# Kernel optimization log

Measured on AMD Instinct MI355X. Metric: run time of the kernel, lower is better.

The kernel has to match this reference:

```python
import jax, jax.numpy as jnp
import numpy as np

DIM = 1024
MLP_RATIO = 4
EPS = 1e-6


def rmsnorm(x, w):
    return x * jax.lax.rsqrt(jnp.mean(x * x, axis=-1, keepdims=True) + EPS) * w


def film(x, cond, w, b):
    # cond: [B, D] -> scale/shift: [B, D] each, broadcast over tokens
    ss = cond @ w + b  # [B, 2D]
    scale, shift = jnp.split(ss, 2, axis=-1)
    return x * (1.0 + scale[:, None, :]) + shift[:, None, :]


def setup_inputs() -> dict:
    key = jax.random.key(0)
    ks = jax.random.split(key, 16)
    B, N, D = 4, 2048, DIM
    H = D * MLP_RATIO
    s = lambda fan_in: 1.0 / np.sqrt(fan_in)
    return {
        "x": jax.random.normal(ks[0], (B, N, D), jnp.float32),
        "cond": jax.random.normal(ks[1], (B, D), jnp.float32),
        "norm1_w": jnp.ones((D,), jnp.float32),
        "film1_w": jax.random.normal(ks[2], (D, 2 * D), jnp.float32) * s(D),
        "film1_b": jnp.zeros((2 * D,), jnp.float32),
        "q_w": jax.random.normal(ks[3], (D, D), jnp.float32) * s(D),
        "q_b": jnp.zeros((D,), jnp.float32),
        "k_w": jax.random.normal(ks[4], (D, D), jnp.float32) * s(D),
        "k_b": jnp.zeros((D,), jnp.float32),
        "v_w": jax.random.normal(ks[5], (D, D), jnp.float32) * s(D),
        "v_b": jnp.zeros((D,), jnp.float32),
        "proj_w": jax.random.normal(ks[6], (D, D), jnp.float32) * s(D),
        "proj_b": jnp.zeros((D,), jnp.float32),
        "norm2_w": jnp.ones((D,), jnp.float32),
        "film2_w": jax.random.normal(ks[7], (D, 2 * D), jnp.float32) * s(D),
        "film2_b": jnp.zeros((2 * D,), jnp.float32),
        "mlp_w1": jax.random.normal(ks[8], (D, H), jnp.float32) * s(D),
        "mlp_b1": jnp.zeros((H,), jnp.float32),
        "mlp_w2": jax.random.normal(ks[9], (H, D), jnp.float32) * s(H),
        "mlp_b2": jnp.zeros((D,), jnp.float32),
    }


def reference(x, cond, norm1_w, film1_w, film1_b, q_w, q_b, k_w, k_b, v_w, v_b,
              proj_w, proj_b, norm2_w, film2_w, film2_b, mlp_w1, mlp_b1,
              mlp_w2, mlp_b2):
    B, N, D = x.shape
    x_in = x
    h = film(rmsnorm(x, norm1_w), cond, film1_w, film1_b)
    Q = h @ q_w + q_b
    K = h @ k_w + k_b
    V = h @ v_w + v_b
    scores = jnp.einsum('bnd,bmd->bnm', Q, K) * (D ** -0.5)  # [B,N,N]
    attn = jax.nn.softmax(scores, axis=-1)
    out = jnp.einsum('bnm,bmd->bnd', attn, V)
    x = x_in + (out @ proj_w + proj_b)
    x_in = x
    h = film(rmsnorm(x, norm2_w), cond, film2_w, film2_b)
    h = jax.nn.gelu(h @ mlp_w1 + mlp_b1, approximate=False) @ mlp_w2 + mlp_b2
    return x_in + h
```

## Files before the change

### kernel.cpp

```cpp
#include <hip/hip_runtime.h>
#include <math.h>

typedef unsigned short u16;
typedef unsigned int u32;
typedef __bf16 bf16;
typedef bf16 bf16x8 __attribute__((ext_vector_type(8)));
typedef float f32x4 __attribute__((ext_vector_type(4)));

#define DEV __device__ __forceinline__
#define MFMA(a, b, c) __builtin_amdgcn_mfma_f32_16x16x32_bf16(a, b, c, 0, 0, 0)

DEV u16 f2b(float f) {
  unsigned u = __builtin_bit_cast(unsigned, f);
  u += 0x7fffu + ((u >> 16) & 1u);
  return (u16)(u >> 16);
}
DEV float b2f(u16 h) {
  unsigned u = ((unsigned)h) << 16;
  return __builtin_bit_cast(float, u);
}
DEV float gelu_f(float x) {
  float e = __expf(x * (-1.5957691216f - 0.07135481283f * x * x));
  return x / (1.0f + e);
}

DEV void gl2lds16(const void* g, void* l) {
  __builtin_amdgcn_global_load_lds(
      (const __attribute__((address_space(1))) unsigned int*)g,
      (__attribute__((address_space(3))) unsigned int*)l, 16, 0, 0);
}

struct TDesc { const float* src; u16* dst; int R, C, t0, tx; };
struct T6 { TDesc d[6]; };

__global__ void k_transpose6(T6 td) {
  __shared__ float tile[32][33];
  const int id = blockIdx.x;
  TDesc d = td.d[0];
#pragma unroll
  for (int k = 1; k < 6; ++k)
    if (id >= td.d[k].t0) d = td.d[k];
  const int local = id - d.t0;
  const int c0 = (local % d.tx) * 32, r0 = (local / d.tx) * 32;
  const int tx = threadIdx.x, ty = threadIdx.y;
#pragma unroll
  for (int i = 0; i < 32; i += 8)
    tile[ty + i][tx] = d.src[(long)(r0 + ty + i) * d.C + c0 + tx];
  __syncthreads();
#pragma unroll
  for (int i = 0; i < 32; i += 8)
    d.dst[(long)(c0 + ty + i) * d.R + r0 + tx] = f2b(tile[tx][ty + i]);
}

__global__ __launch_bounds__(256) void k_film_part(const float* __restrict__ cond,
                                                   const float* __restrict__ f1w,
                                                   const float* __restrict__ f2w,
                                                   float* __restrict__ part) {
  const int j = blockIdx.x * 256 + threadIdx.x;
  const int b = blockIdx.y;
  const int z = blockIdx.z;
  const int kz = z & 7;
  const float* fw = (z < 8) ? f1w : f2w;
  const float* cp = cond + b * 1024 + kz * 128;
  const float* wp = fw + (long)kz * 128 * 2048 + j;
  float acc = 0.0f;
#pragma unroll 4
  for (int d = 0; d < 128; ++d) acc = fmaf(cp[d], wp[(long)d * 2048], acc);
  part[((z * 4 + b) << 11) + j] = acc;
}
__global__ __launch_bounds__(256) void k_film_comb(const float* __restrict__ part,
                                                   const float* __restrict__ f1b,
                                                   const float* __restrict__ f2b_,
                                                   float* __restrict__ ss) {
  const int j = blockIdx.x * 256 + threadIdx.x;
  const int b = blockIdx.y & 3, f = blockIdx.y >> 2;
  float a = (f ? f2b_ : f1b)[j];
#pragma unroll
  for (int kz = 0; kz < 8; ++kz) a += part[(((f * 8 + kz) * 4 + b) << 11) + j];
  ss[((f * 4 + b) << 11) + j] = a;
}

template <typename InT>
__global__ __launch_bounds__(256) void k_rmsfilm(const InT* __restrict__ x,
                                                 const float* __restrict__ nw,
                                                 const float* __restrict__ ss,
                                                 u16* __restrict__ h) {
  const int row = blockIdx.x;
  const int b = row >> 11;
  const int t = threadIdx.x;
  float4 v;
  if constexpr (sizeof(InT) == 4) {
    v = ((const float4*)(x + (long)row * 1024))[t];
  } else {
    ushort4 u = ((const ushort4*)(x + (long)row * 1024))[t];
    v = make_float4(b2f(u.x), b2f(u.y), b2f(u.z), b2f(u.w));
  }
  float s = v.x * v.x + v.y * v.y + v.z * v.z + v.w * v.w;
#pragma unroll
  for (int off = 32; off; off >>= 1) s += __shfl_xor(s, off);
  __shared__ float red[4];
  const int wv = t >> 6, lane = t & 63;
  if (lane == 0) red[wv] = s;
  __syncthreads();
  const float tot = red[0] + red[1] + red[2] + red[3];
  const float rn = rsqrtf(tot * (1.0f / 1024.0f) + 1e-6f);
  const float4 w4 = ((const float4*)nw)[t];
  const float4 sc = ((const float4*)(ss + b * 2048))[t];
  const float4 sh = ((const float4*)(ss + b * 2048 + 1024))[t];
  ushort4 o;
  o.x = f2b(v.x * rn * w4.x * (1.0f + sc.x) + sh.x);
  o.y = f2b(v.y * rn * w4.y * (1.0f + sc.y) + sh.y);
  o.z = f2b(v.z * rn * w4.z * (1.0f + sc.z) + sh.z);
  o.w = f2b(v.w * rn * w4.w * (1.0f + sc.w) + sh.w);
  ((ushort4*)(h + (long)row * 1024))[t] = o;
}

__global__ __launch_bounds__(256) void k_rowsuminv(const float* __restrict__ part,
                                                   float* __restrict__ inv) {
  const int id = blockIdx.x * 256 + threadIdx.x;
  float s = 0.0f;
#pragma unroll
  for (int b = 0; b < 16; ++b) s += part[b * 8192 + id];
  inv[id] = 1.0f / s;
}

enum { EB = 1, ES = 2, EG = 4, ER = 8, EQKV = 16, ERB = 32, EEXP = 64, EPVN = 128 };

template <int BN, int EPI, typename OutT>
__global__ __launch_bounds__(256, 4) void k_gemm(
    const u16* __restrict__ A, const u16* __restrict__ B, OutT* __restrict__ C,
    const float* __restrict__ bias, const float* __restrict__ bias2,
    const float* __restrict__ bias3, const float* __restrict__ resid,
    u16* __restrict__ Vt, float* __restrict__ rsum, float scale,
    int N, int K, long sAb, long sBb, long sCb) {
  constexpr int NR = BN / 32;
  constexpr int NBC = BN * 8 / 256;
  __shared__ u16 As[128 * 64];
  __shared__ u16 Bs[BN * 64];
  const int tid = threadIdx.x, lane = tid & 63, wv = tid >> 6;
  const int wr = wv >> 1, wc = wv & 1;
  const int r = lane & 15, q = lane >> 4;

  const int f = blockIdx.y * gridDim.x + blockIdx.x;
  const int nxy = gridDim.x * gridDim.y;
  const int o = (f & 7) * (nxy >> 3) + (f >> 3);
  const int st = o >> 6, t6 = o & 63;
  const int sxw = gridDim.x >> 3;
  const int bx = (st % sxw) * 8 + (t6 & 7);
  const int by = (st / sxw) * 8 + (t6 >> 3);

  const long bm = (long)by * 128, bn = (long)bx * BN;
  const u16* Ab = A + (long)blockIdx.z * sAb + bm * K;
  const u16* Bb = B + (long)blockIdx.z * sBb + bn * K;

  f32x4 acc[4][NR] = {};

  for (int k0 = 0; k0 < K; k0 += 64) {
#pragma unroll
    for (int i = 0; i < 4; ++i) {
      const int c = i * 256 + tid;
      const int row = c >> 3, sp = c & 7;
      const long g = (long)row * K + k0 + ((sp ^ (row & 7)) << 3);
      gl2lds16(Ab + g, As + c * 8);
    }
#pragma unroll
    for (int i = 0; i < NBC; ++i) {
      const int c = i * 256 + tid;
      const int row = c >> 3, sp = c & 7;
      const long g = (long)row * K + k0 + ((sp ^ (row & 7)) << 3);
      gl2lds16(Bb + g, Bs + c * 8);
    }
    __syncthreads();
    bf16x8 a[8], b[2 * NR];
#pragma unroll
    for (int kh = 0; kh < 2; ++kh) {
#pragma unroll
      for (int i = 0; i < 4; ++i) {
        const int ar = wr * 64 + i * 16 + r;
        a[kh * 4 + i] = *(const bf16x8*)&As[ar * 64 + ((kh * 4 + q) ^ (ar & 7)) * 8];
      }
#pragma unroll
      for (int ni = 0; ni < NR; ++ni) {
        const int br = wc * (BN / 2) + ni * 16 + r;
        b[kh * NR + ni] = *(const bf16x8*)&Bs[br * 64 + ((kh * 4 + q) ^ (br & 7)) * 8];
      }
    }
#pragma unroll
    for (int kh = 0; kh < 2; ++kh)
#pragma unroll
      for (int mi = 0; mi < 4; ++mi)
#pragma unroll
        for (int ni = 0; ni < NR; ++ni)
          acc[mi][ni] = MFMA(a[kh * 4 + mi], b[kh * NR + ni], acc[mi][ni]);
    __syncthreads();
  }

  const long cb = (long)blockIdx.z * sCb;
  constexpr bool VMODE = ((EPI & EQKV) != 0);
  const bool isV = VMODE && (bx >= 16);
  float rs[4][4];
  if constexpr ((EPI & EEXP) != 0) {
#pragma unroll
    for (int mi = 0; mi < 4; ++mi)
#pragma unroll
      for (int j = 0; j < 4; ++j) rs[mi][j] = 0.0f;
  }
  float* lb = (float*)As;

#pragma unroll
  for (int ni = 0; ni < NR; ++ni) {
    const long col = bn + wc * (BN / 2) + ni * 16 + r;
    float bv = 0.0f;
    if constexpr ((EPI & EB) != 0) bv = bias[col];
    if constexpr (VMODE) {
      const int c = (int)col & 1023;
      bv = (bx < 8) ? bias[c] : (bx < 16) ? bias2[c] : bias3[c];
    }
    ushort4 vo[4];
#pragma unroll
    for (int mi = 0; mi < 4; ++mi) {
      float vj[4];
#pragma unroll
      for (int j = 0; j < 4; ++j) {
        float v = acc[mi][ni][j];
        if constexpr ((EPI & ES) != 0) v *= scale;
        if constexpr ((EPI & EEXP) != 0) {
          v = __expf(v * scale);
          rs[mi][j] += v;
        }
        if constexpr ((EPI & EPVN) != 0) {
          const long row = bm + wr * 64 + mi * 16 + q * 4 + j;
          v *= bias[(long)blockIdx.z * 2048 + row];
        }
        v += bv;
        if constexpr ((EPI & EG) != 0) v = gelu_f(v);
        vj[j] = v;
      }
      if constexpr (VMODE) {
        vo[mi].x = f2b(vj[0]); vo[mi].y = f2b(vj[1]);
        vo[mi].z = f2b(vj[2]); vo[mi].w = f2b(vj[3]);
      }
      if (!isV) {
#pragma unroll
        for (int j = 0; j < 4; ++j)
          lb[(wr * 64 + mi * 16 + q * 4 + j) * 32 + wc * 16 + r] = vj[j];
      }
    }
    if constexpr (VMODE) {
      if (isV) {
        const int c = (int)col & 1023;
#pragma unroll
        for (int mi = 0; mi < 4; ++mi) {
          const long row = bm + wr * 64 + mi * 16 + q * 4;
          *(ushort4*)&Vt[((row >> 11) << 21) + ((long)c << 11) + (row & 2047)] = vo[mi];
        }
      }
    }
    __syncthreads();
    if (!isV) {
#pragma unroll
      for (int s = 0; s < 2; ++s) {
        const int ch = s * 256 + tid;
        const int row128 = ch >> 2, cc = ch & 3;
        const long grow = bm + row128;
        const long gcol = bn + (long)(cc >> 1) * (BN / 2) + ni * 16 + (cc & 1) * 8;
        float v8[8];
#pragma unroll
        for (int k = 0; k < 8; ++k) v8[k] = lb[row128 * 32 + cc * 8 + k];
        if constexpr ((EPI & ER) != 0) {
          const float4 r0 = *(const float4*)&resid[grow * N + gcol];
          const float4 r1 = *(const float4*)&resid[grow * N + gcol + 4];
          v8[0] += r0.x; v8[1] += r0.y; v8[2] += r0.z; v8[3] += r0.w;
          v8[4] += r1.x; v8[5] += r1.y; v8[6] += r1.z; v8[7] += r1.w;
        }
        if constexpr ((EPI & ERB) != 0) {
          const ushort4 r0 = *(const ushort4*)&((const u16*)resid)[grow * N + gcol];
          const ushort4 r1 = *(const ushort4*)&((const u16*)resid)[grow * N + gcol + 4];
          v8[0] += b2f(r0.x); v8[1] += b2f(r0.y); v8[2] += b2f(r0.z); v8[3] += b2f(r0.w);
          v8[4] += b2f(r1.x); v8[5] += b2f(r1.y); v8[6] += b2f(r1.z); v8[7] += b2f(r1.w);
        }
        if constexpr (VMODE) {
          u16* dst = (u16*)C + ((bx < 8) ? 0L : 8388608L);
          uint4 o4;
          o4.x = (u32)f2b(v8[0]) | ((u32)f2b(v8[1]) << 16);
          o4.y = (u32)f2b(v8[2]) | ((u32)f2b(v8[3]) << 16);
          o4.z = (u32)f2b(v8[4]) | ((u32)f2b(v8[5]) << 16);
          o4.w = (u32)f2b(v8[6]) | ((u32)f2b(v8[7]) << 16);
          *(uint4*)&dst[grow * 1024 + (gcol & 1023)] = o4;
        } else if constexpr (sizeof(OutT) == 4) {
          float4 f0 = {v8[0], v8[1], v8[2], v8[3]};
          float4 f1 = {v8[4], v8[5], v8[6], v8[7]};
          *(float4*)&C[cb + grow * N + gcol] = f0;
          *(float4*)&C[cb + grow * N + gcol + 4] = f1;
        } else {
          uint4 o4;
          o4.x = (u32)f2b(v8[0]) | ((u32)f2b(v8[1]) << 16);
          o4.y = (u32)f2b(v8[2]) | ((u32)f2b(v8[3]) << 16);
          o4.z = (u32)f2b(v8[4]) | ((u32)f2b(v8[5]) << 16);
          o4.w = (u32)f2b(v8[6]) | ((u32)f2b(v8[7]) << 16);
          *(uint4*)&((u16*)C)[cb + grow * N + gcol] = o4;
        }
      }
    }
    __syncthreads();
  }

  if constexpr ((EPI & EEXP) != 0) {
    float* rbuf = (float*)As;
#pragma unroll
    for (int mi = 0; mi < 4; ++mi)
#pragma unroll
      for (int j = 0; j < 4; ++j) {
        float v = rs[mi][j];
        v += __shfl_xor(v, 1);
        v += __shfl_xor(v, 2);
        v += __shfl_xor(v, 4);
        v += __shfl_xor(v, 8);
        rs[mi][j] = v;
      }
    __syncthreads();
    if (r == 0) {
#pragma unroll
      for (int mi = 0; mi < 4; ++mi)
#pragma unroll
        for (int j = 0; j < 4; ++j)
          rbuf[wc * 128 + wr * 64 + mi * 16 + q * 4 + j] = rs[mi][j];
    }
    __syncthreads();
    if (tid < 128) {
      const float s = rbuf[tid] + rbuf[128 + tid];
      rsum[(long)bx * 8192 + (long)blockIdx.z * 2048 + bm + tid] = s;
    }
  }
  (void)Vt; (void)rsum; (void)bias2; (void)bias3; (void)resid;
}

extern "C" void kernel_launch(void* const* d_in, const int* in_sizes, int n_in,
                              void* d_out, int out_size, void* d_ws, size_t ws_size,
                              hipStream_t stream) {
  const float* x    = (const float*)d_in[0];
  const float* cond = (const float*)d_in[1];
  const float* n1w  = (const float*)d_in[2];
  const float* f1w  = (const float*)d_in[3];
  const float* f1b  = (const float*)d_in[4];
  const float* qw   = (const float*)d_in[5];
  const float* qb   = (const float*)d_in[6];
  const float* kw   = (const float*)d_in[7];
  const float* kb   = (const float*)d_in[8];
  const float* vw   = (const float*)d_in[9];
  const float* vb   = (const float*)d_in[10];
  const float* pw   = (const float*)d_in[11];
  const float* pb   = (const float*)d_in[12];
  const float* n2w  = (const float*)d_in[13];
  const float* f2w  = (const float*)d_in[14];
  const float* f2b_ = (const float*)d_in[15];
  const float* w1   = (const float*)d_in[16];
  const float* b1   = (const float*)d_in[17];
  const float* w2   = (const float*)d_in[18];
  const float* b2   = (const float*)d_in[19];
  float* out = (float*)d_out;

  char* ws = (char*)d_ws;
  size_t o = 0;
  auto alloc = [&](size_t bytes) {
    size_t ret = o;
    o += (bytes + 255) & ~(size_t)255;
    return ret;
  };
  const long N = 2048, D = 1024, H = 4096;

  u16* qkvT = (u16*)(ws + alloc(3 * D * D * 2));
  u16* pT   = (u16*)(ws + alloc(D * D * 2));
  u16* w1T  = (u16*)(ws + alloc(D * H * 2));
  u16* w2T  = (u16*)(ws + alloc(D * H * 2));
  float* ss    = (float*)(ws + alloc(2 * 4 * 2 * D * 4));
  float* part  = (float*)(ws + alloc(16 * 4 * 2 * D * 4));
  float* spart = (float*)(ws + alloc(16 * 8192 * 4));
  float* rsinv = (float*)(ws + alloc(8192 * 4));
  u16* h    = (u16*)(ws + alloc(4 * N * D * 2));
  u16* x1b  = (u16*)(ws + alloc(4 * N * D * 2));
  u16* AO   = (u16*)(ws + alloc(4 * N * D * 2));
  const size_t big = o;
  u16* Q    = (u16*)(ws + alloc(4 * N * D * 2));
  u16* Kb   = (u16*)(ws + alloc(4 * N * D * 2));
  u16* Vt   = (u16*)(ws + alloc(4 * N * D * 2));
  u16* S    = (u16*)(ws + alloc(4 * N * N * 2));
  u16* h1   = (u16*)(ws + big);
  (void)ws_size; (void)in_sizes; (void)n_in; (void)out_size; (void)Kb;

  T6 td;
  td.d[0] = {qw, qkvT,                1024, 1024,    0,  32};
  td.d[1] = {kw, qkvT + 1024 * 1024,  1024, 1024, 1024,  32};
  td.d[2] = {vw, qkvT + 2048 * 1024,  1024, 1024, 2048,  32};
  td.d[3] = {pw, pT,                  1024, 1024, 3072,  32};
  td.d[4] = {w1, w1T,                 1024, 4096, 4096, 128};
  td.d[5] = {w2, w2T,                 4096, 1024, 8192,  32};
  k_transpose6<<<12288, dim3(32, 8), 0, stream>>>(td);

  k_film_part<<<dim3(8, 4, 16), 256, 0, stream>>>(cond, f1w, f2w, part);
  k_film_comb<<<dim3(8, 8), 256, 0, stream>>>(part, f1b, f2b_, ss);

  k_rmsfilm<float><<<8192, 256, 0, stream>>>(x, n1w, ss, h);

  k_gemm<128, EQKV, u16><<<dim3(24, 64, 1), 256, 0, stream>>>(
      h, qkvT, Q, qb, kb, vb, nullptr, Vt, nullptr, 1.0f, 3072, 1024, 0, 0, 0);

  k_gemm<128, EEXP, u16><<<dim3(16, 16, 4), 256, 0, stream>>>(
      Q, Kb, S, nullptr, nullptr, nullptr, nullptr, nullptr, spart, 0.03125f,
      2048, 1024, N * D, N * D, N * N);
  k_rowsuminv<<<32, 256, 0, stream>>>(spart, rsinv);

  k_gemm<64, EPVN, u16><<<dim3(16, 16, 4), 256, 0, stream>>>(
      S, Vt, AO, rsinv, nullptr, nullptr, nullptr, nullptr, nullptr, 1.0f,
      1024, 2048, N * N, D * N, N * D);

  k_gemm<64, EB | ER, u16><<<dim3(16, 64, 1), 256, 0, stream>>>(
      AO, pT, x1b, pb, nullptr, nullptr, x, nullptr, nullptr, 1.0f, 1024, 1024, 0, 0, 0);

  k_rmsfilm<u16><<<8192, 256, 0, stream>>>(x1b, n2w, ss + 4 * 2048, h);

  k_gemm<128, EB | EG, u16><<<dim3(32, 64, 1), 256, 0, stream>>>(
      h, w1T, h1, b1, nullptr, nullptr, nullptr, nullptr, nullptr, 1.0f, 4096, 1024, 0, 0, 0);

  k_gemm<64, EB | ERB, float><<<dim3(16, 64, 1), 256, 0, stream>>>(
      h1, w2T, out, b2, nullptr, nullptr, (const float*)x1b, nullptr, nullptr, 1.0f,
      1024, 4096, 0, 0, 0);
}
```

Baseline: 378.9 us.

## Double-buffer GEMM LDS tiles with BK=32 to overlap loads and MFMA

The generic GEMM kernel moves from a single-buffered 64-wide K tile to two 32-wide LDS buffers. The next tile's global-to-LDS copy is issued before the MFMAs on the current tile, and the XOR swizzle is reworked for 32-element rows. The goal is to hide global load latency behind compute while keeping total LDS the same. The cost is twice as many barriers and loop iterations per K, and the async copies may not actually overlap if the load instruction waits on completion.

```diff
diff --git a/kernel.cpp b/kernel.cpp
--- a/kernel.cpp
+++ b/kernel.cpp
@@ -134,9 +134,11 @@
     u16* __restrict__ Vt, float* __restrict__ rsum, float scale,
     int N, int K, long sAb, long sBb, long sCb) {
   constexpr int NR = BN / 32;
-  constexpr int NBC = BN * 8 / 256;
-  __shared__ u16 As[128 * 64];
-  __shared__ u16 Bs[BN * 64];
+  constexpr int NBC = BN / 64;
+  constexpr int ASZ = 128 * 32;
+  constexpr int BSZ = BN * 32;
+  __shared__ u16 As[2 * ASZ];
+  __shared__ u16 Bs[2 * BSZ];
   const int tid = threadIdx.x, lane = tid & 63, wv = tid >> 6;
   const int wr = wv >> 1, wc = wv & 1;
   const int r = lane & 15, q = lane >> 4;
@@ -153,46 +155,47 @@
   const u16* Ab = A + (long)blockIdx.z * sAb + bm * K;
   const u16* Bb = B + (long)blockIdx.z * sBb + bn * K;
 
-  f32x4 acc[4][NR] = {};
-
-  for (int k0 = 0; k0 < K; k0 += 64) {
-#pragma unroll
-    for (int i = 0; i < 4; ++i) {
+  auto stage = [&](int buf, int k0) {
+#pragma unroll
+    for (int i = 0; i < 2; ++i) {
       const int c = i * 256 + tid;
-      const int row = c >> 3, sp = c & 7;
-      const long g = (long)row * K + k0 + ((sp ^ (row & 7)) << 3);
-      gl2lds16(Ab + g, As + c * 8);
+      const int row = c >> 2, sp = c & 3;
+      const long g = (long)row * K + k0 + ((sp ^ ((row >> 1) & 3)) << 3);
+      gl2lds16(Ab + g, As + buf * ASZ + c * 8);
     }
 #pragma unroll
     for (int i = 0; i < NBC; ++i) {
       const int c = i * 256 + tid;
-      const int row = c >> 3, sp = c & 7;
-      const long g = (long)row * K + k0 + ((sp ^ (row & 7)) << 3);
-      gl2lds16(Bb + g, Bs + c * 8);
-    }
+      const int row = c >> 2, sp = c & 3;
+      const long g = (long)row * K + k0 + ((sp ^ ((row >> 1) & 3)) << 3);
+      gl2lds16(Bb + g, Bs + buf * BSZ + c * 8);
+    }
+  };
+
+  f32x4 acc[4][NR] = {};
+
+  stage(0, 0);
+  __syncthreads();
+  int cur = 0;
+  const int cs = (q ^ ((r >> 1) & 3)) * 8;
+  for (int k0 = 0; k0 < K; k0 += 32) {
+    if (k0 + 32 < K) stage(cur ^ 1, k0 + 32);
+    const u16* Ac = As + cur * ASZ;
+    const u16* Bc = Bs + cur * BSZ;
+    bf16x8 a[4], b[NR];
+#pragma unroll
+    for (int i = 0; i < 4; ++i)
+      a[i] = *(const bf16x8*)&Ac[(wr * 64 + i * 16 + r) * 32 + cs];
+#pragma unroll
+    for (int ni = 0; ni < NR; ++ni)
+      b[ni] = *(const bf16x8*)&Bc[(wc * (BN / 2) + ni * 16 + r) * 32 + cs];
+#pragma unroll
+    for (int mi = 0; mi < 4; ++mi)
+#pragma unroll
+      for (int ni = 0; ni < NR; ++ni)
+        acc[mi][ni] = MFMA(a[mi], b[ni], acc[mi][ni]);
     __syncthreads();
-    bf16x8 a[8], b[2 * NR];
-#pragma unroll
-    for (int kh = 0; kh < 2; ++kh) {
-#pragma unroll
-      for (int i = 0; i < 4; ++i) {
-        const int ar = wr * 64 + i * 16 + r;
-        a[kh * 4 + i] = *(const bf16x8*)&As[ar * 64 + ((kh * 4 + q) ^ (ar & 7)) * 8];
-      }
-#pragma unroll
-      for (int ni = 0; ni < NR; ++ni) {
-        const int br = wc * (BN / 2) + ni * 16 + r;
-        b[kh * NR + ni] = *(const bf16x8*)&Bs[br * 64 + ((kh * 4 + q) ^ (br & 7)) * 8];
-      }
-    }
-#pragma unroll
-    for (int kh = 0; kh < 2; ++kh)
-#pragma unroll
-      for (int mi = 0; mi < 4; ++mi)
-#pragma unroll
-        for (int ni = 0; ni < NR; ++ni)
-          acc[mi][ni] = MFMA(a[kh * 4 + mi], b[kh * NR + ni], acc[mi][ni]);
-    __syncthreads();
+    cur ^= 1;
   }
 
   const long cb = (long)blockIdx.z * sCb;
```

Result: slower. 460.0 us (+21.4%).
